# Kernel tuning notes

Measured on AMD Instinct MI355X. Metric: run time of the kernel, lower is better.

Reference implementation:

```python
import jax, jax.numpy as jnp
import numpy as np

DIM, NH, NKV, HD = 4096, 32, 8, 128
N_REP = NH // NKV
START_POS = 32767  # decode position; cache holds positions [0, START_POS)


def _rope(x, cos, sin):
    # x: (B, L, H, D); cos/sin: (L, D/2). Complex multiply on (even, odd) pairs.
    b, l, h, d = x.shape
    xr = x.reshape(b, l, h, d // 2, 2)
    x0, x1 = xr[..., 0], xr[..., 1]
    c = cos[None, :, None, :]
    s = sin[None, :, None, :]
    o0 = x0 * c - x1 * s
    o1 = x0 * s + x1 * c
    return jnp.stack([o0, o1], axis=-1).reshape(b, l, h, d)


def setup_inputs() -> dict:
    key = jax.random.key(0)
    ks = jax.random.split(key, 8)
    x = jax.random.normal(ks[0], (1, 1, DIM), jnp.float32)
    # real RoPE angles for the current position
    inv_freq = 1.0 / (10000.0 ** (np.arange(0, HD, 2, dtype=np.float32) / HD))
    ang = jnp.asarray((START_POS * inv_freq)[None, :], jnp.float32)  # (1, 64)
    freqs_cos = jnp.cos(ang)
    freqs_sin = jnp.sin(ang)
    k_cache = jax.random.normal(ks[1], (START_POS, NKV, HD), jnp.float32)
    v_cache = jax.random.normal(ks[2], (START_POS, NKV, HD), jnp.float32)
    sd = 1.0 / np.sqrt(DIM)
    wq = jax.random.normal(ks[3], (NH * HD, DIM), jnp.float32) * sd
    wk = jax.random.normal(ks[4], (NKV * HD, DIM), jnp.float32) * sd
    wv = jax.random.normal(ks[5], (NKV * HD, DIM), jnp.float32) * sd
    wo = jax.random.normal(ks[6], (DIM, NH * HD), jnp.float32) * sd
    return {"x": x, "freqs_cos": freqs_cos, "freqs_sin": freqs_sin,
            "k_cache": k_cache, "v_cache": v_cache,
            "wq": wq, "wk": wk, "wv": wv, "wo": wo,
            "start_pos": START_POS}


def reference(x, freqs_cos, freqs_sin, k_cache, v_cache, wq, wk, wv, wo, start_pos):
    bsz, seqlen, _ = x.shape  # (1, 1, DIM)
    q = (x @ wq.T).reshape(bsz, seqlen, NH, HD)
    k = (x @ wk.T).reshape(bsz, seqlen, NKV, HD)
    v = (x @ wv.T).reshape(bsz, seqlen, NKV, HD)
    q = _rope(q, freqs_cos, freqs_sin)
    k = _rope(k, freqs_cos, freqs_sin)
    # push current token KV and fetch full history (offloader fetch over all
    # blocks 0..start_pos//BLOCK == plain concat of cache + current token)
    k_full = jnp.concatenate([k_cache, k[0]], axis=0)  # (T, NKV, HD), T = start_pos+1
    v_full = jnp.concatenate([v_cache, v[0]], axis=0)
    # GQA repeat_kv: (T, NKV, HD) -> (1, NH, T, HD)
    T = k_full.shape[0]
    k_h = jnp.repeat(k_full, N_REP, axis=1).transpose(1, 0, 2)[None]  # (1, NH, T, HD)
    v_h = jnp.repeat(v_full, N_REP, axis=1).transpose(1, 0, 2)[None]
    qh = q.transpose(0, 2, 1, 3)  # (1, NH, 1, HD)
    scores = jnp.einsum("bhqd,bhtd->bhqt", qh, k_h) / jnp.sqrt(jnp.float32(HD))
    probs = jax.nn.softmax(scores, axis=-1)
    out = jnp.einsum("bhqt,bhtd->bhqd", probs, v_h)  # (1, NH, 1, HD)
    out = out.transpose(0, 2, 1, 3).reshape(bsz, seqlen, NH * HD)
    return out @ wo.T
```

## Files before the change

kernel.cpp:

```cpp
#include <hip/hip_runtime.h>
#include <math.h>

#define DIM 4096
#define NH 32
#define NKV 8
#define HD 128
#define NREP 4
#define NSPLIT 256

typedef float f32x4 __attribute__((ext_vector_type(4)));

__global__ __launch_bounds__(256) void qkv_rope_kernel(
    const float* __restrict__ x, const float* __restrict__ fc,
    const float* __restrict__ fs, const float* __restrict__ wq,
    const float* __restrict__ wk, const float* __restrict__ wv,
    float* __restrict__ q_rope, float* __restrict__ k_new,
    float* __restrict__ v_new, float* __restrict__ attn_raw) {
  if (blockIdx.x == 0) {
    for (int i = threadIdx.x; i < NH * HD + NH; i += 256) attn_raw[i] = 0.f;
  }
  int wave = blockIdx.x * 4 + (threadIdx.x >> 6);
  int lane = threadIdx.x & 63;
  const float* W;
  float* dst;
  int r0;
  bool rope;
  if (wave < 2048) {
    W = wq; dst = q_rope; r0 = wave * 2; rope = true;
  } else if (wave < 2560) {
    W = wk; dst = k_new; r0 = (wave - 2048) * 2; rope = true;
  } else {
    W = wv; dst = v_new; r0 = (wave - 2560) * 2; rope = false;
  }
  const float4* x4 = (const float4*)x;
  const float4* w0 = (const float4*)(W + (size_t)r0 * DIM);
  const float4* w1 = (const float4*)(W + (size_t)(r0 + 1) * DIM);
  float a0 = 0.f, a1 = 0.f;
#pragma unroll 4
  for (int c = lane; c < DIM / 4; c += 64) {
    float4 xv = x4[c];
    float4 u = w0[c];
    float4 v = w1[c];
    a0 += xv.x * u.x + xv.y * u.y + xv.z * u.z + xv.w * u.w;
    a1 += xv.x * v.x + xv.y * v.y + xv.z * v.z + xv.w * v.w;
  }
  for (int off = 32; off > 0; off >>= 1) {
    a0 += __shfl_down(a0, off, 64);
    a1 += __shfl_down(a1, off, 64);
  }
  if (lane == 0) {
    if (rope) {
      int j = (r0 & (HD - 1)) >> 1;
      float c = fc[j], s = fs[j];
      dst[r0]     = a0 * c - a1 * s;
      dst[r0 + 1] = a0 * s + a1 * c;
    } else {
      dst[r0]     = a0;
      dst[r0 + 1] = a1;
    }
  }
}

#define LD4(p) (*(const float4*)(p))
#define NT4(p) (__builtin_nontemporal_load((const f32x4*)(p)))

#define DOT4(sv, h)                                                         \
  sv = A.x * qf[h][0] + A.y * qf[h][1] + A.z * qf[h][2] + A.w * qf[h][3] +  \
       B.x * qf[h][4] + B.y * qf[h][5] + B.z * qf[h][6] + B.w * qf[h][7];

#define PV8(h, e)                                                           \
  acc[h][0] += (e)*VA.x; acc[h][1] += (e)*VA.y;                             \
  acc[h][2] += (e)*VA.z; acc[h][3] += (e)*VA.w;                             \
  acc[h][4] += (e)*VB.x; acc[h][5] += (e)*VB.y;                             \
  acc[h][6] += (e)*VB.z; acc[h][7] += (e)*VB.w;

#define STEP(KA_, KB_, VA_, VB_, VALID)                                     \
  {                                                                         \
    auto A = KA_; auto B = KB_;                                             \
    float s0, s1, s2, s3;                                                   \
    DOT4(s0, 0); DOT4(s1, 1); DOT4(s2, 2); DOT4(s3, 3);                     \
    float pp = hi8 ? s2 : s0, pq = hi8 ? s0 : s2;                           \
    pp += __shfl_xor(pq, 8, 64);                                            \
    float rr = hi8 ? s3 : s1, rs = hi8 ? s1 : s3;                           \
    rr += __shfl_xor(rs, 8, 64);                                            \
    float u = hi4 ? rr : pp, uvx = hi4 ? pp : rr;                           \
    u += __shfl_xor(uvx, 4, 64);                                            \
    u += __shfl_xor(u, 1, 64);                                              \
    u += __shfl_xor(u, 2, 64);                                              \
    float u4 = __shfl_xor(u, 4, 64);                                        \
    float u8 = __shfl_xor(u, 8, 64);                                        \
    float u12 = __shfl_xor(u4, 8, 64);                                      \
    float q0 = hi4 ? u4 : u,   q1 = hi4 ? u : u4;                           \
    float q2 = hi4 ? u12 : u8, q3 = hi4 ? u8 : u12;                         \
    float w0 = hi8 ? q2 : q0, w1 = hi8 ? q3 : q1;                           \
    float w2 = hi8 ? q0 : q2, w3 = hi8 ? q1 : q3;                           \
    float e0 = __expf((VALID) ? w0 * scale : -1e30f);                       \
    float e1 = __expf((VALID) ? w1 * scale : -1e30f);                       \
    float e2 = __expf((VALID) ? w2 * scale : -1e30f);                       \
    float e3 = __expf((VALID) ? w3 * scale : -1e30f);                       \
    lsum[0] += e0; lsum[1] += e1; lsum[2] += e2; lsum[3] += e3;             \
    auto VA = VA_; auto VB = VB_;                                           \
    PV8(0, e0) PV8(1, e1) PV8(2, e2) PV8(3, e3)                             \
  }

__global__ __launch_bounds__(256, 4) void attn_partial_kernel(
    const float* __restrict__ q_rope, const float* __restrict__ k_cache,
    const float* __restrict__ v_cache, const float* __restrict__ k_new,
    const float* __restrict__ v_new, float* __restrict__ attn_raw,
    float* __restrict__ L_raw, int start_pos, int T, int CH) {
  int g0 = (blockIdx.x & 3) * 2;
  int split = blockIdx.x >> 2;
  int t0 = split * CH;
  int tid = threadIdx.x;
  int wvi = tid >> 6;
  int lane = tid & 63;
  int grp = lane >> 4;
  int lig = lane & 15;
  int gsel = grp & 1;
  int g = g0 + gsel;
  int tl0 = wvi * 2 + (grp >> 1);
  int dbase = lig * 8;
  bool hi8 = (lig & 8) != 0, hi4 = (lig & 4) != 0;

  __shared__ float s_wacc[4][2][NREP][HD];
  __shared__ float s_wl[4][2][NREP];

  float qf[4][8];
#pragma unroll
  for (int h = 0; h < 4; ++h)
#pragma unroll
    for (int e = 0; e < 8; ++e)
      qf[h][e] = q_rope[(g * NREP + h) * HD + dbase + e];

  float lsum[4] = {0.f, 0.f, 0.f, 0.f};
  float acc[4][8];
#pragma unroll
  for (int h = 0; h < 4; ++h)
#pragma unroll
    for (int e = 0; e < 8; ++e) acc[h][e] = 0.f;

  const float scale = 0.08838834764831845f;
  int iters = CH >> 3;
  bool full = (t0 + CH + 8 <= start_pos);
  const size_t kstep = (size_t)8 * NKV * HD;

  if (full) {
    const float* kp = k_cache + ((size_t)(t0 + tl0) * NKV + g) * HD + dbase;
    const float* vp = v_cache + ((size_t)(t0 + tl0) * NKV + g) * HD + dbase;
    f32x4 KA0 = NT4(kp), KB0 = NT4(kp + 4);
    f32x4 VA0 = NT4(vp), VB0 = NT4(vp + 4);
    kp += kstep; vp += kstep;
    for (int i = 0; i < iters; i += 2) {
      f32x4 KA1 = NT4(kp), KB1 = NT4(kp + 4);
      f32x4 VA1 = NT4(vp), VB1 = NT4(vp + 4);
      kp += kstep; vp += kstep;
      __builtin_amdgcn_sched_barrier(0);
      STEP(KA0, KB0, VA0, VB0, true);
      KA0 = NT4(kp); KB0 = NT4(kp + 4);
      VA0 = NT4(vp); VB0 = NT4(vp + 4);
      kp += kstep; vp += kstep;
      __builtin_amdgcn_sched_barrier(0);
      STEP(KA1, KB1, VA1, VB1, true);
    }
  } else {
    for (int i = 0; i < iters; ++i) {
      int t = t0 + i * 8 + tl0;
      bool valid = (t < T);
      const float* kp;
      const float* vp;
      if (t < start_pos) {
        kp = k_cache + ((size_t)t * NKV + g) * HD;
        vp = v_cache + ((size_t)t * NKV + g) * HD;
      } else {
        kp = k_new + (size_t)g * HD;
        vp = v_new + (size_t)g * HD;
      }
      f32x4 KA = NT4(kp + dbase), KB = NT4(kp + dbase + 4);
      f32x4 VAx = NT4(vp + dbase), VBx = NT4(vp + dbase + 4);
      STEP(KA, KB, VAx, VBx, valid);
    }
  }

#pragma unroll
  for (int h = 0; h < 4; ++h) {
    lsum[h] += __shfl_xor(lsum[h], 32, 64);
#pragma unroll
    for (int e = 0; e < 8; ++e) acc[h][e] += __shfl_xor(acc[h][e], 32, 64);
  }
  if (grp < 2) {
#pragma unroll
    for (int h = 0; h < 4; ++h)
#pragma unroll
      for (int e = 0; e < 8; ++e)
        s_wacc[wvi][gsel][h][dbase + e] = acc[h][e];
    if (lig == 0) {
#pragma unroll
      for (int h = 0; h < 4; ++h) s_wl[wvi][gsel][h] = lsum[h];
    }
  }
  __syncthreads();
  for (int o = tid; o < 2 * NREP * HD; o += 256) {
    int gs = o >> 9, h = (o >> 7) & 3, d = o & (HD - 1);
    float sum = s_wacc[0][gs][h][d] + s_wacc[1][gs][h][d] +
                s_wacc[2][gs][h][d] + s_wacc[3][gs][h][d];
    atomicAdd(&attn_raw[((g0 + gs) * NREP + h) * HD + d], sum);
  }
  if (tid < 2 * NREP) {
    int gs = tid >> 2, h = tid & 3;
    atomicAdd(&L_raw[(g0 + gs) * NREP + h],
              s_wl[0][gs][h] + s_wl[1][gs][h] + s_wl[2][gs][h] +
                  s_wl[3][gs][h]);
  }
}

__global__ __launch_bounds__(256) void out_gemv_kernel(
    const float* __restrict__ attn_raw, const float* __restrict__ L_raw,
    const float* __restrict__ wo, float* __restrict__ out) {
  __shared__ float s_invL[NH];
  if (threadIdx.x < NH) s_invL[threadIdx.x] = 1.f / L_raw[threadIdx.x];
  __syncthreads();
  int row = blockIdx.x * 4 + (threadIdx.x >> 6);
  int lane = threadIdx.x & 63;
  const float4* a4 = (const float4*)attn_raw;
  const float4* w4 = (const float4*)(wo + (size_t)row * DIM);
  float a = 0.f;
#pragma unroll 4
  for (int c = lane; c < DIM / 4; c += 64) {
    float4 av = a4[c];
    float4 wv = w4[c];
    float il = s_invL[c >> 5];
    a += (av.x * wv.x + av.y * wv.y + av.z * wv.z + av.w * wv.w) * il;
  }
  for (int off = 32; off > 0; off >>= 1) a += __shfl_down(a, off, 64);
  if (lane == 0) out[row] = a;
}

extern "C" void kernel_launch(void* const* d_in, const int* in_sizes, int n_in,
                              void* d_out, int out_size, void* d_ws,
                              size_t ws_size, hipStream_t stream) {
  const float* x       = (const float*)d_in[0];
  const float* fc      = (const float*)d_in[1];
  const float* fs      = (const float*)d_in[2];
  const float* k_cache = (const float*)d_in[3];
  const float* v_cache = (const float*)d_in[4];
  const float* wq      = (const float*)d_in[5];
  const float* wk      = (const float*)d_in[6];
  const float* wv      = (const float*)d_in[7];
  const float* wo      = (const float*)d_in[8];
  float* out = (float*)d_out;

  int start_pos = in_sizes[3] / (NKV * HD);
  int T = start_pos + 1;
  int CH = ((T + NSPLIT - 1) / NSPLIT + 7) & ~7;

  float* ws = (float*)d_ws;
  float* q_rope   = ws;
  float* k_new    = ws + 4096;
  float* v_new    = ws + 5120;
  float* attn_raw = ws + 6144;
  float* L_raw    = attn_raw + NH * HD;

  qkv_rope_kernel<<<768, 256, 0, stream>>>(x, fc, fs, wq, wk, wv, q_rope,
                                           k_new, v_new, attn_raw);
  attn_partial_kernel<<<4 * NSPLIT, 256, 0, stream>>>(
      q_rope, k_cache, v_cache, k_new, v_new, attn_raw, L_raw,
      start_pos, T, CH);
  out_gemv_kernel<<<1024, 256, 0, stream>>>(attn_raw, L_raw, wo, out);
}
```

Measured before the change: 88.88 us.

## Remap attention blocks so each covers all KV heads over a contiguous token chunk

Each attention block previously handled two KV heads over eight token rows. Now one block covers all eight KV heads for a contiguous chunk of tokens: each 16-lane group takes one head, and waves split tokens by parity. Every block therefore reads whole contiguous cache rows (8 heads × 128 floats), which should improve DRAM locality and remove the cross-half shuffle reduction. In exchange each block does more atomics per split (all 32 heads' outputs), the grid has the same block count but with a different work shape, and the chunk per block is smaller.

After: 94.04 us. 1.06x slower.

```diff
diff --git a/kernel.cpp b/kernel.cpp
--- a/kernel.cpp
+++ b/kernel.cpp
@@ -6,7 +6,7 @@
 #define NKV 8
 #define HD 128
 #define NREP 4
-#define NSPLIT 256
+#define NSPLIT 1024
 
 typedef float f32x4 __attribute__((ext_vector_type(4)));
 
@@ -108,22 +108,21 @@
     const float* __restrict__ v_cache, const float* __restrict__ k_new,
     const float* __restrict__ v_new, float* __restrict__ attn_raw,
     float* __restrict__ L_raw, int start_pos, int T, int CH) {
-  int g0 = (blockIdx.x & 3) * 2;
-  int split = blockIdx.x >> 2;
+  int split = blockIdx.x;
   int t0 = split * CH;
   int tid = threadIdx.x;
   int wvi = tid >> 6;
   int lane = tid & 63;
   int grp = lane >> 4;
   int lig = lane & 15;
-  int gsel = grp & 1;
-  int g = g0 + gsel;
-  int tl0 = wvi * 2 + (grp >> 1);
+  int ghalf = wvi & 1;
+  int pparity = wvi >> 1;
+  int g = ghalf * 4 + grp;
   int dbase = lig * 8;
   bool hi8 = (lig & 8) != 0, hi4 = (lig & 4) != 0;
 
-  __shared__ float s_wacc[4][2][NREP][HD];
-  __shared__ float s_wl[4][2][NREP];
+  __shared__ float s_wacc[4][4][NREP][HD];
+  __shared__ float s_wl[4][4][NREP];
 
   float qf[4][8];
 #pragma unroll
@@ -140,13 +139,13 @@
     for (int e = 0; e < 8; ++e) acc[h][e] = 0.f;
 
   const float scale = 0.08838834764831845f;
-  int iters = CH >> 3;
-  bool full = (t0 + CH + 8 <= start_pos);
-  const size_t kstep = (size_t)8 * NKV * HD;
+  int iters = CH >> 1;
+  bool full = (t0 + CH + 2 <= start_pos);
+  const size_t kstep = (size_t)2 * NKV * HD;
 
   if (full) {
-    const float* kp = k_cache + ((size_t)(t0 + tl0) * NKV + g) * HD + dbase;
-    const float* vp = v_cache + ((size_t)(t0 + tl0) * NKV + g) * HD + dbase;
+    const float* kp = k_cache + ((size_t)(t0 + pparity) * NKV + g) * HD + dbase;
+    const float* vp = v_cache + ((size_t)(t0 + pparity) * NKV + g) * HD + dbase;
     f32x4 KA0 = NT4(kp), KB0 = NT4(kp + 4);
     f32x4 VA0 = NT4(vp), VB0 = NT4(vp + 4);
     kp += kstep; vp += kstep;
@@ -164,7 +163,7 @@
     }
   } else {
     for (int i = 0; i < iters; ++i) {
-      int t = t0 + i * 8 + tl0;
+      int t = t0 + i * 2 + pparity;
       bool valid = (t < T);
       const float* kp;
       const float* vp;
@@ -182,34 +181,25 @@
   }
 
 #pragma unroll
-  for (int h = 0; h < 4; ++h) {
-    lsum[h] += __shfl_xor(lsum[h], 32, 64);
-#pragma unroll
-    for (int e = 0; e < 8; ++e) acc[h][e] += __shfl_xor(acc[h][e], 32, 64);
-  }
-  if (grp < 2) {
-#pragma unroll
-    for (int h = 0; h < 4; ++h)
-#pragma unroll
-      for (int e = 0; e < 8; ++e)
-        s_wacc[wvi][gsel][h][dbase + e] = acc[h][e];
-    if (lig == 0) {
-#pragma unroll
-      for (int h = 0; h < 4; ++h) s_wl[wvi][gsel][h] = lsum[h];
-    }
+  for (int h = 0; h < 4; ++h)
+#pragma unroll
+    for (int e = 0; e < 8; ++e) s_wacc[wvi][grp][h][dbase + e] = acc[h][e];
+  if (lig == 0) {
+#pragma unroll
+    for (int h = 0; h < 4; ++h) s_wl[wvi][grp][h] = lsum[h];
   }
   __syncthreads();
-  for (int o = tid; o < 2 * NREP * HD; o += 256) {
-    int gs = o >> 9, h = (o >> 7) & 3, d = o & (HD - 1);
-    float sum = s_wacc[0][gs][h][d] + s_wacc[1][gs][h][d] +
-                s_wacc[2][gs][h][d] + s_wacc[3][gs][h][d];
-    atomicAdd(&attn_raw[((g0 + gs) * NREP + h) * HD + d], sum);
-  }
-  if (tid < 2 * NREP) {
-    int gs = tid >> 2, h = tid & 3;
-    atomicAdd(&L_raw[(g0 + gs) * NREP + h],
-              s_wl[0][gs][h] + s_wl[1][gs][h] + s_wl[2][gs][h] +
-                  s_wl[3][gs][h]);
+  for (int o = tid; o < NKV * NREP * HD; o += 256) {
+    int gg = o >> 9, h = (o >> 7) & 3, d = o & (HD - 1);
+    int gh = gg >> 2, gr = gg & 3;
+    float sum = s_wacc[gh][gr][h][d] + s_wacc[gh + 2][gr][h][d];
+    atomicAdd(&attn_raw[(gg * NREP + h) * HD + d], sum);
+  }
+  if (tid < NKV * NREP) {
+    int gg = tid >> 2, h = tid & 3;
+    int gh = gg >> 2, gr = gg & 3;
+    atomicAdd(&L_raw[gg * NREP + h],
+              s_wl[gh][gr][h] + s_wl[gh + 2][gr][h]);
   }
 }
 
@@ -251,7 +241,7 @@
 
   int start_pos = in_sizes[3] / (NKV * HD);
   int T = start_pos + 1;
-  int CH = ((T + NSPLIT - 1) / NSPLIT + 7) & ~7;
+  int CH = ((T + NSPLIT - 1) / NSPLIT + 1) & ~1;
 
   float* ws = (float*)d_ws;
   float* q_rope   = ws;
@@ -262,7 +252,7 @@
 
   qkv_rope_kernel<<<768, 256, 0, stream>>>(x, fc, fs, wq, wk, wv, q_rope,
                                            k_new, v_new, attn_raw);
-  attn_partial_kernel<<<4 * NSPLIT, 256, 0, stream>>>(
+  attn_partial_kernel<<<NSPLIT, 256, 0, stream>>>(
       q_rope, k_cache, v_cache, k_new, v_new, attn_raw, L_raw,
       start_pos, T, CH);
   out_gemv_kernel<<<1024, 256, 0, stream>>>(attn_raw, L_raw, wo, out);
```
